# Kernel optimization log

Measured on AMD Instinct MI355X. Metric: run time of the kernel, lower is better.

## Reference

```python
import jax, jax.numpy as jnp
import numpy as np

PRE_NMS_TOP_K = 6000   # 'test' mode
POST_NMS_TOP_K = 300   # 'test' mode
IOU_THRESHOLD = 0.7


def setup_inputs() -> dict:
    key = jax.random.key(0)
    k1, k2, k3, k4 = jax.random.split(key, 4)
    B, A, H, W = 1, 9, 64, 96
    N = H * W * A  # 55296 anchors
    pred_cls = jax.random.normal(k1, (B, 2 * A, H, W), dtype=jnp.float32)
    pred_loc = jax.random.normal(k2, (B, 4 * A, H, W), dtype=jnp.float32) * 0.1
    # anchors in normalized (cx, cy, w, h) format
    cxcy = jax.random.uniform(k3, (N, 2), dtype=jnp.float32)
    wh = jax.random.uniform(k4, (N, 2), dtype=jnp.float32) * 0.2 + 0.02
    anchor = jnp.concatenate([cxcy, wh], axis=-1)
    return {"pred_cls": pred_cls, "pred_loc": pred_loc, "anchor": anchor}


def _decode_to_xy(loc, anchor):
    # decode: t(cx,cy) * a(w,h) + a(cx,cy); exp(t(w,h)) * a(w,h); then cxcy -> xyxy
    cxcy = loc[:, :2] * anchor[:, 2:] + anchor[:, :2]
    wh = jnp.exp(loc[:, 2:]) * anchor[:, 2:]
    return jnp.concatenate([cxcy - wh * 0.5, cxcy + wh * 0.5], axis=-1)


def _iou_matrix(boxes):
    # boxes: [N,4] xyxy -> [N,N] IoU
    area = (boxes[:, 2] - boxes[:, 0]) * (boxes[:, 3] - boxes[:, 1])
    lt = jnp.maximum(boxes[:, None, :2], boxes[None, :, :2])  # [N,N,2]
    rb = jnp.minimum(boxes[:, None, 2:], boxes[None, :, 2:])  # [N,N,2]
    wh = jnp.clip(rb - lt, 0.0)
    inter = wh[..., 0] * wh[..., 1]
    union = area[:, None] + area[None, :] - inter
    return inter / jnp.maximum(union, 1e-12)


def _nms_keep(boxes, iou_threshold):
    # boxes already sorted by descending score -> greedy NMS
    n = boxes.shape[0]
    iou = _iou_matrix(boxes)
    idx = jnp.arange(n)

    def body(i, keep):
        suppress = (iou[i] > iou_threshold) & (idx > i)
        return jnp.where(keep[i], keep & ~suppress, keep)

    return jax.lax.fori_loop(0, n, body, jnp.ones((n,), dtype=bool))


def reference(pred_cls, pred_loc, anchor):
    B = pred_cls.shape[0]
    # NCHW -> NHWC -> [N, 2] / [N, 4]  (batch squeezed, B == 1)
    cls = jnp.transpose(pred_cls, (0, 2, 3, 1)).reshape(B, -1, 2)[0]
    loc = jnp.transpose(pred_loc, (0, 2, 3, 1)).reshape(B, -1, 4)[0]

    roi = jnp.clip(_decode_to_xy(loc, anchor), 0.0, 1.0)           # [N,4]
    scores = jax.nn.sigmoid(cls)[:, 1]                              # [N]

    order = jnp.argsort(-scores)[:PRE_NMS_TOP_K]                    # descending
    roi = roi[order]                                                # [K,4]

    keep = _nms_keep(roi, IOU_THRESHOLD)                            # [K] bool
    # kept boxes first (stable -> preserves score order), take top 300
    sel = jnp.argsort(jnp.where(keep, 0, 1), stable=True)[:POST_NMS_TOP_K]
    valid = keep[sel]
    # pad with zeros if fewer than 300 boxes survive NMS (torch returns a
    # dynamically-sized tensor; we keep a fixed [300,4] with zero padding)
    return jnp.where(valid[:, None], roi[sel], 0.0)
```

## Files before the change

### kernel.cpp

```cpp
#include <hip/hip_runtime.h>


#define ADIM 9
#define NANCH 55296
#define HWSZ 6144
#define CH_U4 1536
#define TOT_U4 13824
#define TOPK 6000
#define OUTK 300
#define NBINS 16384
#define CAP 8192
#define SCAP 1024
#define SRANK 133
#define MROWS 512
#define MW 8
#define THR 0.7f

typedef unsigned long long u64;
typedef unsigned int u32;

__device__ __forceinline__ u32 flipu(u32 b) {
    u32 u = (b & 0x80000000u) ? ~b : (b | 0x80000000u);
    return ~u;
}

__device__ __forceinline__ bool iou_gt(float4 a, float aa, float4 b, float ba) {
    float ix = fminf(a.z, b.z) - fmaxf(a.x, b.x);
    float iy = fminf(a.w, b.w) - fmaxf(a.y, b.y);
    float inter = fmaxf(ix, 0.f) * fmaxf(iy, 0.f);
    float u = fmaxf(aa + ba - inter, 1e-12f);
    float d = __builtin_fmaf(-THR, u, inter);
    if (__builtin_fabsf(d) > 1e-6f * u) return d > 0.f;
    return inter / u > THR;
}

__device__ __forceinline__ float4 decode_box(const float* __restrict__ loc,
                                             const float* __restrict__ anc, u32 n) {
    u32 a = n % 9u, hw = n / 9u;
    float t0 = loc[(4 * a + 0) * HWSZ + hw];
    float t1 = loc[(4 * a + 1) * HWSZ + hw];
    float t2 = loc[(4 * a + 2) * HWSZ + hw];
    float t3 = loc[(4 * a + 3) * HWSZ + hw];
    float4 an = reinterpret_cast<const float4*>(anc)[n];
    float cx = t0 * an.z + an.x;
    float cy = t1 * an.w + an.y;
    float bw = expf(t2) * an.z;
    float bh = expf(t3) * an.w;
    return make_float4(fminf(fmaxf(cx - bw * 0.5f, 0.f), 1.f),
                       fminf(fmaxf(cy - bh * 0.5f, 0.f), 1.f),
                       fminf(fmaxf(cx + bw * 0.5f, 0.f), 1.f),
                       fminf(fmaxf(cy + bh * 0.5f, 0.f), 1.f));
}

__device__ __forceinline__ u64 sx64(u64 v, int m) {
    u32 lo = __shfl_xor((u32)(v & 0xffffffffu), m, 64);
    u32 hi = __shfl_xor((u32)(v >> 32), m, 64);
    return ((u64)hi << 32) | lo;
}

__device__ __forceinline__ u64 ce64(u64 v, int j, int lane, bool up) {
    u64 pv = sx64(v, j);
    u64 mn = (pv < v) ? pv : v;
    u64 mx = (pv < v) ? v : pv;
    return (((lane & j) == 0) == up) ? mn : mx;
}

__device__ __forceinline__ uint4 ld_cls4(const uint4* __restrict__ cls4, int i) {
    int ch = i / CH_U4;
    int e4 = i - ch * CH_U4;
    return cls4[(2 * ch + 1) * CH_U4 + e4];
}

__device__ __forceinline__ u32 block_scan(u32 s, int wid, int lane, u32* wsum) {
    u32 x = s;
    #pragma unroll
    for (int d = 1; d < 64; d <<= 1) {
        u32 y = __shfl_up(x, (unsigned)d, 64);
        if (lane >= d) x += y;
    }
    if (lane == 63) wsum[wid] = x;
    __syncthreads();
    if (wid == 0) {
        u32 w = (lane < 16) ? wsum[lane] : 0u;
        #pragma unroll
        for (int d = 1; d < 16; d <<= 1) {
            u32 y = __shfl_up(w, (unsigned)d, 64);
            if (lane >= d) w += y;
        }
        if (lane < 16) wsum[lane] = w;
    }
    __syncthreads();
    return x + (wid ? wsum[wid - 1] : 0u);
}

__device__ __forceinline__ u32 find_cutoff(const u32* hist, u32 thresh, int tid,
                                           int wid, int lane, u32* wsum, u32* sB) {
    u32 h[16];
    const uint4* h4 = reinterpret_cast<const uint4*>(hist);
    #pragma unroll
    for (int k = 0; k < 4; ++k) {
        uint4 v = h4[tid * 4 + k];
        h[4 * k + 0] = v.x; h[4 * k + 1] = v.y; h[4 * k + 2] = v.z; h[4 * k + 3] = v.w;
    }
    u32 s = 0;
    #pragma unroll
    for (int b = 0; b < 16; ++b) s += h[b];
    u32 incl = block_scan(s, wid, lane, wsum);
    u32 before = incl - s;
    if (before < thresh && incl >= thresh) {
        u32 run = before;
        #pragma unroll
        for (int b = 0; b < 16; ++b) {
            run += h[b];
            if (run >= thresh) { sB[0] = (u32)(tid * 16 + b); break; }
        }
    }
    __syncthreads();
    u32 r = sB[0];
    __syncthreads();
    return r;
}

__global__ void __launch_bounds__(1024) k_scanrank(const float* __restrict__ cls,
                                                   const float* __restrict__ loc,
                                                   const float* __restrict__ anc,
                                                   u32* __restrict__ wsMeta,
                                                   float4* __restrict__ boxS,
                                                   float* __restrict__ areaS) {
    __shared__ u32 hist[NBINS];
    __shared__ u64 skey[SCAP];
    __shared__ u32 wsum[16];
    __shared__ u32 sB[2];
    __shared__ u32 shu[2];

    const int tid = threadIdx.x;
    const int wid = tid >> 6;
    const int lane = tid & 63;
    const uint4* cls4 = reinterpret_cast<const uint4*>(cls);

    u64* h64 = (u64*)hist;
    for (int i = tid; i < NBINS / 2; i += 1024) h64[i] = 0ull;
    if (tid < 2) shu[tid] = 0;
    __syncthreads();

    uint4 buf[14];
    #pragma unroll
    for (int kk = 0; kk < 14; ++kk) {
        int i = kk * 1024 + tid;
        buf[kk] = (i < TOT_U4) ? ld_cls4(cls4, i)
                               : make_uint4(0xFF800000u, 0xFF800000u, 0xFF800000u, 0xFF800000u);
    }
    #pragma unroll
    for (int kk = 0; kk < 14; ++kk)
        atomicAdd(&hist[flipu(buf[kk].x) >> 18], 1u);
    __syncthreads();
    const u32 B1 = find_cutoff(hist, SRANK, tid, wid, lane, wsum, sB);
    const u32 K1 = (B1 + 1u) << 18;

    u64 bm = 0;
    u32 cnt = 0;
    #pragma unroll
    for (int kk = 0; kk < 14; ++kk) {
        int i = kk * 1024 + tid;
        if (i < TOT_U4) {
            #pragma unroll
            for (int c = 0; c < 4; ++c) {
                u32 b = (c == 0) ? buf[kk].x : (c == 1) ? buf[kk].y
                      : (c == 2) ? buf[kk].z : buf[kk].w;
                if (flipu(b) < K1) {
                    cnt++;
                    bm |= 1ull << (kk * 4 + c);
                }
            }
        }
    }
    u32 incl = block_scan(cnt, wid, lane, wsum);
    u32 base = incl - cnt;
    if (tid == 1023) shu[0] = incl;
    __syncthreads();
    const u32 csRaw = shu[0];
    const u32 cs = csRaw < SCAP ? csRaw : SCAP;
    if (blockIdx.x == 0 && tid == 0) { wsMeta[0] = csRaw; wsMeta[1] = B1; }
    if (csRaw > SCAP) return;

    {
        u64 m = bm;
        u32 o = base;
        while (m) {
            int b = __ffsll((unsigned long long)m) - 1;
            m &= m - 1;
            int kk = b >> 2, c = b & 3;
            int i = kk * 1024 + tid;
            uint4 v = ld_cls4(cls4, i);
            u32 raw = (c == 0) ? v.x : (c == 1) ? v.y : (c == 2) ? v.z : v.w;
            int ch = i / CH_U4;
            int e4 = i - ch * CH_U4;
            u32 n = (u32)((e4 * 4 + c) * ADIM + ch);
            if (o < SCAP) skey[o] = ((u64)flipu(raw) << 32) | n;
            o++;
        }
    }
    if (tid >= (int)cs) skey[tid] = ~0ull;
    __syncthreads();

    const int ci = blockIdx.x * 64 + (tid >> 4);
    const int p = tid & 15;
    const u64 myk = skey[ci];
    u32 r = 0;
    #pragma unroll 8
    for (int k = 0; k < 64; ++k) {
        int j = k * 16 + p;
        r += (skey[j] < myk) ? 1u : 0u;
    }
    r += __shfl_xor(r, 1, 64);
    r += __shfl_xor(r, 2, 64);
    r += __shfl_xor(r, 4, 64);
    r += __shfl_xor(r, 8, 64);
    if (p == 0 && (u32)ci < csRaw) {
        float4 b = decode_box(loc, anc, (u32)myk);
        boxS[r] = b;
        areaS[r] = (b.z - b.x) * (b.w - b.y);
    }
}

__global__ void __launch_bounds__(1024) k_mat(const u32* __restrict__ wsMeta,
                                              const float4* __restrict__ boxS,
                                              const float* __restrict__ areaS,
                                              u32* __restrict__ maskG32,
                                              float4* __restrict__ out) {
    __shared__ float4 B[MROWS];
    __shared__ float  A[MROWS];
    __shared__ u32 M32[32][16];
    const int tid = threadIdx.x;
    if (blockIdx.x == 0 && tid < OUTK)
        out[tid] = make_float4(0.f, 0.f, 0.f, 0.f);
    const u32 csRaw = wsMeta[0];
    if (csRaw > SCAP) return;
    const u32 rowsv = csRaw < MROWS ? csRaw : MROWS;

    if (tid < MROWS) { B[tid] = boxS[tid]; A[tid] = areaS[tid]; }
    if (tid < 512) M32[tid >> 4][tid & 15] = 0u;
    __syncthreads();

    const int rl = tid >> 5;
    const int sub = tid & 31;
    const int row = blockIdx.x + 16 * rl;
    if (row < (int)rowsv) {
        const int j0 = sub * 16;
        int jmax = row < j0 + 16 ? row : j0 + 16;
        if (j0 < jmax) {
            float4 rb = B[row];
            float rba = A[row];
            u32 bits = 0;
            #pragma unroll 4
            for (int j = j0; j < jmax; ++j)
                if (iou_gt(rb, rba, B[j], A[j])) bits |= 1u << (j - j0);
            if (bits) atomicOr(&M32[rl][sub >> 1], bits << ((sub & 1) * 16));
        }
    }
    __syncthreads();
    if (tid < 512) {
        int rl2 = tid >> 4, w = tid & 15;
        int row2 = blockIdx.x + 16 * rl2;
        maskG32[row2 * 16 + w] = M32[rl2][w];
    }
}

__global__ void __launch_bounds__(1024) k_greedy(const float* __restrict__ cls,
                                                 const float* __restrict__ loc,
                                                 const float* __restrict__ anc,
                                                 const u32* __restrict__ wsMeta,
                                                 const float4* __restrict__ boxS,
                                                 const float* __restrict__ areaS,
                                                 const u32* __restrict__ maskG32,
                                                 float4* __restrict__ out) {
    __shared__ u64 cand[CAP];
    __shared__ u64 smask[MROWS][MW];
    __shared__ float4 sbox[SCAP];
    __shared__ float  sarea[SCAP];
    __shared__ float4 kept[OUTK];
    __shared__ float  karea[OUTK];
    __shared__ float4 cbox[64];
    __shared__ float  carea[64];
    __shared__ u64 supw[16];
    __shared__ u64 sbyp[1024];
    __shared__ u32 wsum[16];
    __shared__ u32 sB[2];
    __shared__ u32 shu[8];

    const int tid = threadIdx.x;
    const int wid = tid >> 6;
    const int lane = tid & 63;
    u32* hist = (u32*)cand;
    const uint4* cls4 = reinterpret_cast<const uint4*>(cls);

    const u32 csRaw = wsMeta[0];
    const u32 cs = csRaw < SCAP ? csRaw : SCAP;
    const bool fast = (csRaw <= SCAP);

    if (tid < 8) shu[tid] = 0;
    sbox[tid] = boxS[tid];
    sarea[tid] = areaS[tid];
    {
        u32* sm32 = (u32*)smask;
        #pragma unroll
        for (int k = 0; k < 8; ++k) sm32[k * 1024 + tid] = maskG32[k * 1024 + tid];
    }
    __syncthreads();

    if (fast) {
        const u32 rowsv = cs < MROWS ? cs : MROWS;
        if (wid == 0) {
            u32 kc = 0, nexti0 = 0;
            u64 K[MW];
            #pragma unroll
            for (int w = 0; w < MW; ++w) K[w] = 0ull;
            #pragma unroll
            for (int cw = 0; cw < MW; ++cw) {
                u32 i0 = (u32)cw * 64u;
                if (i0 < rowsv && kc < OUTK) {
                    u32 ci = i0 + (u32)lane;
                    bool valid = ci < rowsv;
                    u64 myw[MW];
                    #pragma unroll
                    for (int w = 0; w < MW; ++w) myw[w] = valid ? smask[ci][w] : 0ull;
                    u64 supk = 0;
                    #pragma unroll
                    for (int w = 0; w < MW; ++w) supk |= myw[w] & K[w];
                    bool ia = valid && (supk == 0ull);
                    u64 inch = myw[cw] & ((1ull << lane) - 1ull);
                    u64 A = __ballot(ia ? 1 : 0);
                    for (int itx = 0; itx < 64; ++itx) {
                        bool na = ia && ((inch & A) == 0ull);
                        u64 A2 = __ballot(na ? 1 : 0);
                        if (A2 == A) break;
                        A = A2;
                    }
                    bool kp = (A >> lane) & 1;
                    u32 rank = (u32)__popcll(A & ((1ull << lane) - 1ull));
                    if (kp && kc + rank < OUTK) {
                        float4 c = sbox[ci];
                        kept[kc + rank] = c;
                        karea[kc + rank] = sarea[ci];
                        out[kc + rank] = c;
                    }
                    K[cw] = A;
                    kc += (u32)__popcll(A);
                    nexti0 = i0 + 64;
                }
            }
            if (lane == 0) {
                shu[4] = kc > OUTK ? OUTK : kc;
                shu[5] = nexti0;
            }
        }

        const u32 limit = cs;
        while (true) {
            __syncthreads();
            u32 kc = shu[4], i0 = shu[5];
            if (kc >= OUTK || i0 >= limit) break;
            u32 ci = i0 + (u32)lane;
            bool valid = ci < limit;
            float4 c = sbox[valid ? ci : 0];
            float ca = sarea[valid ? ci : 0];

            bool sup = false;
            for (u32 j = (u32)wid; j < kc; j += 16)
                sup = sup || iou_gt(c, ca, kept[j], karea[j]);
            u64 bal = __ballot(sup ? 1 : 0);
            if (lane == 0) supw[wid] = bal;

            u64 sby = 0;
            u32 smax = 4u * wid + 4u; if (smax > 63u) smax = 63u;
            for (u32 s = 4u * wid + 1u; s <= smax; ++s) {
                u32 p = ((u32)lane + s) & 63u;
                if (p < (u32)lane && (i0 + p) < limit)
                    if (iou_gt(c, ca, sbox[i0 + p], sarea[i0 + p])) sby |= (1ull << p);
            }
            sbyp[wid * 64 + lane] = sby;
            __syncthreads();

            if (wid == 0) {
                u64 sup64 = 0, sbyfull = 0;
                #pragma unroll
                for (int w = 0; w < 16; ++w) { sup64 |= supw[w]; sbyfull |= sbyp[w * 64 + lane]; }
                bool ia = valid && !((sup64 >> lane) & 1);
                u64 A = __ballot(ia ? 1 : 0);
                for (int itx = 0; itx < 64; ++itx) {
                    bool na = ia && ((sbyfull & A) == 0);
                    u64 A2 = __ballot(na ? 1 : 0);
                    if (A2 == A) break;
                    A = A2;
                }
                bool kp = (A >> lane) & 1;
                u32 rank = (u32)__popcll(A & ((1ull << lane) - 1ull));
                if (kp && kc + rank < OUTK) {
                    kept[kc + rank] = c; karea[kc + rank] = ca; out[kc + rank] = c;
                }
                if (lane == 0) {
                    u32 nk = kc + (u32)__popcll(A);
                    shu[4] = nk > OUTK ? OUTK : nk;
                    shu[5] = i0 + 64;
                }
            }
        }
    }

    __syncthreads();
    if (shu[4] < OUTK) {
        const u32 consumed = fast ? cs : 0u;
        u64* h64 = (u64*)hist;
        for (int i = tid; i < NBINS / 2; i += 1024) h64[i] = 0ull;
        __syncthreads();
        #pragma unroll
        for (int half = 0; half < 2; ++half) {
            uint4 buf[7];
            #pragma unroll
            for (int kk = 0; kk < 7; ++kk) {
                int i = (half * 7 + kk) * 1024 + tid;
                buf[kk] = (i < TOT_U4) ? ld_cls4(cls4, i) : make_uint4(0u,0u,0u,0u);
            }
            #pragma unroll
            for (int kk = 0; kk < 7; ++kk) {
                int i = (half * 7 + kk) * 1024 + tid;
                if (i < TOT_U4) {
                    atomicAdd(&hist[flipu(buf[kk].x) >> 18], 1u);
                    atomicAdd(&hist[flipu(buf[kk].y) >> 18], 1u);
                    atomicAdd(&hist[flipu(buf[kk].z) >> 18], 1u);
                    atomicAdd(&hist[flipu(buf[kk].w) >> 18], 1u);
                }
            }
        }
        __syncthreads();
        const u32 B2 = find_cutoff(hist, TOPK, tid, wid, lane, wsum, sB);
        u64 bm2 = 0;
        u32 cnt2 = 0;
        #pragma unroll
        for (int half = 0; half < 2; ++half) {
            uint4 buf[7];
            #pragma unroll
            for (int kk = 0; kk < 7; ++kk) {
                int i = (half * 7 + kk) * 1024 + tid;
                buf[kk] = (i < TOT_U4) ? ld_cls4(cls4, i) : make_uint4(0xFFFFFFFFu,0xFFFFFFFFu,0xFFFFFFFFu,0xFFFFFFFFu);
            }
            #pragma unroll
            for (int kk = 0; kk < 7; ++kk) {
                int i = (half * 7 + kk) * 1024 + tid;
                if (i < TOT_U4) {
                    #pragma unroll
                    for (int c = 0; c < 4; ++c) {
                        u32 b = (c == 0) ? buf[kk].x : (c == 1) ? buf[kk].y
                              : (c == 2) ? buf[kk].z : buf[kk].w;
                        if ((flipu(b) >> 18) <= B2) {
                            cnt2++;
                            bm2 |= 1ull << ((half * 7 + kk) * 4 + c);
                        }
                    }
                }
            }
        }
        __syncthreads();
        for (int i = tid; i < CAP; i += 1024) cand[i] = ~0ull;
        u32 incl2 = block_scan(cnt2, wid, lane, wsum);
        u32 base2 = incl2 - cnt2;
        if (tid == 1023) shu[1] = incl2;
        __syncthreads();
        {
            u64 m2 = bm2;
            u32 o = base2;
            while (m2) {
                int b = __ffsll((unsigned long long)m2) - 1;
                m2 &= m2 - 1;
                int kk = b >> 2, c = b & 3;
                int i = kk * 1024 + tid;
                uint4 v = ld_cls4(cls4, i);
                u32 raw = (c == 0) ? v.x : (c == 1) ? v.y : (c == 2) ? v.z : v.w;
                int ch = i / CH_U4;
                int e4 = i - ch * CH_U4;
                u32 n = (u32)((e4 * 4 + c) * ADIM + ch);
                if (o < CAP) cand[o] = ((u64)flipu(raw) << 32) | n;
                o++;
            }
        }
        __syncthreads();
        const u32 totF = shu[1];
        const u32 limfb = totF < TOPK ? totF : TOPK;
        for (int seg = wid; seg < CAP / 64; seg += 16) {
            u64 v = cand[seg * 64 + lane];
            #pragma unroll
            for (int k = 2; k <= 64; k <<= 1)
                #pragma unroll
                for (int j = k >> 1; j >= 1; j >>= 1)
                    v = ce64(v, j, lane, (((seg * 64 + lane) & k) == 0));
            cand[seg * 64 + lane] = v;
        }
        __syncthreads();
        for (int k = 128; k <= CAP; k <<= 1) {
            for (int j = k >> 1; j >= 64; j >>= 1) {
                for (u32 p = (u32)tid; p < CAP / 2; p += 1024) {
                    u32 i = ((p & ~(u32)(j - 1)) << 1) | (p & (u32)(j - 1));
                    u32 l = i | (u32)j;
                    bool up = ((i & (u32)k) == 0);
                    u64 a = cand[i], b = cand[l];
                    if ((a > b) == up) { cand[i] = b; cand[l] = a; }
                }
                __syncthreads();
            }
            for (int seg = wid; seg < CAP / 64; seg += 16) {
                u64 v = cand[seg * 64 + lane];
                bool up = (((seg * 64) & k) == 0);
                #pragma unroll
                for (int j = 32; j >= 1; j >>= 1) v = ce64(v, j, lane, up);
                cand[seg * 64 + lane] = v;
            }
            __syncthreads();
        }
        if (tid == 0) shu[5] = consumed;
        while (true) {
            __syncthreads();
            u32 kc = shu[4], i0 = shu[5];
            if (kc >= OUTK || i0 >= limfb) break;
            if (wid == 0) {
                u32 ci = i0 + (u32)lane;
                u32 n = (ci < limfb) ? (u32)cand[ci] : 0u;
                float4 b = decode_box(loc, anc, n);
                cbox[lane] = b;
                carea[lane] = (b.z - b.x) * (b.w - b.y);
            }
            __syncthreads();
            u32 ci = i0 + (u32)lane;
            bool valid = ci < limfb;
            float4 c = cbox[lane];
            float ca = carea[lane];
            bool sup = false;
            for (u32 j = (u32)wid; j < kc; j += 16)
                sup = sup || iou_gt(c, ca, kept[j], karea[j]);
            u64 bal = __ballot(sup ? 1 : 0);
            if (lane == 0) supw[wid] = bal;
            u64 sby = 0;
            u32 smax = 4u * wid + 4u; if (smax > 63u) smax = 63u;
            for (u32 s = 4u * wid + 1u; s <= smax; ++s) {
                u32 p = ((u32)lane + s) & 63u;
                if (p < (u32)lane && (i0 + p) < limfb)
                    if (iou_gt(c, ca, cbox[p], carea[p])) sby |= (1ull << p);
            }
            sbyp[wid * 64 + lane] = sby;
            __syncthreads();
            if (wid == 0) {
                u64 sup64 = 0, sbyfull = 0;
                #pragma unroll
                for (int w = 0; w < 16; ++w) { sup64 |= supw[w]; sbyfull |= sbyp[w * 64 + lane]; }
                bool ia = valid && !((sup64 >> lane) & 1);
                u64 A = __ballot(ia ? 1 : 0);
                for (int itx = 0; itx < 64; ++itx) {
                    bool na = ia && ((sbyfull & A) == 0);
                    u64 A2 = __ballot(na ? 1 : 0);
                    if (A2 == A) break;
                    A = A2;
                }
                bool kp = (A >> lane) & 1;
                u32 rank = (u32)__popcll(A & ((1ull << lane) - 1ull));
                if (kp && kc + rank < OUTK) {
                    kept[kc + rank] = c; karea[kc + rank] = ca; out[kc + rank] = c;
                }
                if (lane == 0) {
                    u32 nk = kc + (u32)__popcll(A);
                    shu[4] = nk > OUTK ? OUTK : nk;
                    shu[5] = i0 + 64;
                }
            }
        }
        __syncthreads();
        u32 kcF2 = shu[4];
        for (u32 r = (u32)tid; r < OUTK; r += 1024)
            if (r >= kcF2) out[r] = make_float4(0.f, 0.f, 0.f, 0.f);
    }
}

extern "C" void kernel_launch(void* const* d_in, const int* in_sizes, int n_in,
                              void* d_out, int out_size, void* d_ws, size_t ws_size,
                              hipStream_t stream) {
    const float* cls = (const float*)d_in[0];
    const float* loc = (const float*)d_in[1];
    const float* anc = (const float*)d_in[2];

    char* ws = (char*)d_ws;
    u32*    wsMeta  = (u32*)(ws + 0);
    float4* boxS    = (float4*)(ws + 16);
    float*  areaS   = (float*)(ws + 16400);
    u32*    maskG32 = (u32*)(ws + 20496);

    k_scanrank<<<16, 1024, 0, stream>>>(cls, loc, anc, wsMeta, boxS, areaS);
    k_mat     <<<16, 1024, 0, stream>>>(wsMeta, boxS, areaS, maskG32, (float4*)d_out);
    k_greedy  <<<1, 1024, 0, stream>>>(cls, loc, anc, wsMeta, boxS, areaS, maskG32, (float4*)d_out);
}
```

Measured before the change: 30.30 us.

## Fuse IoU-mask and greedy kernels with an atomic-counter inter-block handoff

Merges the IoU mask kernel and the single-block greedy kernel into one launch. Blocks 0-15 build the mask and then increment a global counter. The extra greedy block preloads boxes and spin-waits on that counter before reading the mask. This removes one kernel launch boundary and lets the greedy block's setup overlap with mask construction. In exchange it relies on all 17 blocks being co-resident to avoid deadlock, and it adds atomic traffic and spin-polling.

```diff
diff --git a/kernel.cpp b/kernel.cpp
--- a/kernel.cpp
+++ b/kernel.cpp
@@ -15,6 +15,7 @@
 #define MROWS 512
 #define MW 8
 #define THR 0.7f
+#define NMAT 16
 
 typedef unsigned long long u64;
 typedef unsigned int u32;
@@ -180,7 +181,9 @@
     __syncthreads();
     const u32 csRaw = shu[0];
     const u32 cs = csRaw < SCAP ? csRaw : SCAP;
-    if (blockIdx.x == 0 && tid == 0) { wsMeta[0] = csRaw; wsMeta[1] = B1; }
+    if (blockIdx.x == 0 && tid == 0) {
+        wsMeta[0] = csRaw; wsMeta[1] = B1; wsMeta[2] = 0u;
+    }
     if (csRaw > SCAP) return;
 
     {
@@ -223,57 +226,14 @@
     }
 }
 
-__global__ void __launch_bounds__(1024) k_mat(const u32* __restrict__ wsMeta,
-                                              const float4* __restrict__ boxS,
-                                              const float* __restrict__ areaS,
-                                              u32* __restrict__ maskG32,
-                                              float4* __restrict__ out) {
-    __shared__ float4 B[MROWS];
-    __shared__ float  A[MROWS];
-    __shared__ u32 M32[32][16];
-    const int tid = threadIdx.x;
-    if (blockIdx.x == 0 && tid < OUTK)
-        out[tid] = make_float4(0.f, 0.f, 0.f, 0.f);
-    const u32 csRaw = wsMeta[0];
-    if (csRaw > SCAP) return;
-    const u32 rowsv = csRaw < MROWS ? csRaw : MROWS;
-
-    if (tid < MROWS) { B[tid] = boxS[tid]; A[tid] = areaS[tid]; }
-    if (tid < 512) M32[tid >> 4][tid & 15] = 0u;
-    __syncthreads();
-
-    const int rl = tid >> 5;
-    const int sub = tid & 31;
-    const int row = blockIdx.x + 16 * rl;
-    if (row < (int)rowsv) {
-        const int j0 = sub * 16;
-        int jmax = row < j0 + 16 ? row : j0 + 16;
-        if (j0 < jmax) {
-            float4 rb = B[row];
-            float rba = A[row];
-            u32 bits = 0;
-            #pragma unroll 4
-            for (int j = j0; j < jmax; ++j)
-                if (iou_gt(rb, rba, B[j], A[j])) bits |= 1u << (j - j0);
-            if (bits) atomicOr(&M32[rl][sub >> 1], bits << ((sub & 1) * 16));
-        }
-    }
-    __syncthreads();
-    if (tid < 512) {
-        int rl2 = tid >> 4, w = tid & 15;
-        int row2 = blockIdx.x + 16 * rl2;
-        maskG32[row2 * 16 + w] = M32[rl2][w];
-    }
-}
-
-__global__ void __launch_bounds__(1024) k_greedy(const float* __restrict__ cls,
-                                                 const float* __restrict__ loc,
-                                                 const float* __restrict__ anc,
-                                                 const u32* __restrict__ wsMeta,
-                                                 const float4* __restrict__ boxS,
-                                                 const float* __restrict__ areaS,
-                                                 const u32* __restrict__ maskG32,
-                                                 float4* __restrict__ out) {
+__global__ void __launch_bounds__(1024) k_matgreedy(const float* __restrict__ cls,
+                                                    const float* __restrict__ loc,
+                                                    const float* __restrict__ anc,
+                                                    u32* __restrict__ wsMeta,
+                                                    const float4* __restrict__ boxS,
+                                                    const float* __restrict__ areaS,
+                                                    u32* __restrict__ maskG32,
+                                                    float4* __restrict__ out) {
     __shared__ u64 cand[CAP];
     __shared__ u64 smask[MROWS][MW];
     __shared__ float4 sbox[SCAP];
@@ -298,13 +258,62 @@
     const u32 cs = csRaw < SCAP ? csRaw : SCAP;
     const bool fast = (csRaw <= SCAP);
 
+    if (blockIdx.x < NMAT) {
+        if (blockIdx.x == 0 && tid < OUTK)
+            out[tid] = make_float4(0.f, 0.f, 0.f, 0.f);
+        if (fast) {
+            const u32 rowsv = csRaw < MROWS ? csRaw : MROWS;
+            u32* M32 = (u32*)sbyp;
+            if (tid < MROWS) { sbox[tid] = boxS[tid]; sarea[tid] = areaS[tid]; }
+            if (tid < 512) M32[tid] = 0u;
+            __syncthreads();
+            const int rl = tid >> 5;
+            const int sub = tid & 31;
+            const int row = blockIdx.x + 16 * rl;
+            if (row < (int)rowsv) {
+                const int j0 = sub * 16;
+                int jmax = row < j0 + 16 ? row : j0 + 16;
+                if (j0 < jmax) {
+                    float4 rb = sbox[row];
+                    float rba = sarea[row];
+                    u32 bits = 0;
+                    #pragma unroll 4
+                    for (int j = j0; j < jmax; ++j)
+                        if (iou_gt(rb, rba, sbox[j], sarea[j])) bits |= 1u << (j - j0);
+                    if (bits) atomicOr(&M32[rl * 16 + (sub >> 1)], bits << ((sub & 1) * 16));
+                }
+            }
+            __syncthreads();
+            if (tid < 512) {
+                int rl2 = tid >> 4, w = tid & 15;
+                int row2 = blockIdx.x + 16 * rl2;
+                __hip_atomic_store(&maskG32[row2 * 16 + w], M32[rl2 * 16 + w],
+                                   __ATOMIC_RELAXED, __HIP_MEMORY_SCOPE_AGENT);
+            }
+        }
+        __syncthreads();
+        if (tid == 0) {
+            __threadfence();
+            __hip_atomic_fetch_add(&wsMeta[2], 1u, __ATOMIC_RELEASE, __HIP_MEMORY_SCOPE_AGENT);
+        }
+        return;
+    }
+
     if (tid < 8) shu[tid] = 0;
     sbox[tid] = boxS[tid];
     sarea[tid] = areaS[tid];
+    if (tid == 0) {
+        u32 v;
+        do { v = __hip_atomic_load(&wsMeta[2], __ATOMIC_ACQUIRE, __HIP_MEMORY_SCOPE_AGENT); }
+        while (v < (u32)NMAT);
+    }
+    __syncthreads();
     {
         u32* sm32 = (u32*)smask;
         #pragma unroll
-        for (int k = 0; k < 8; ++k) sm32[k * 1024 + tid] = maskG32[k * 1024 + tid];
+        for (int k = 0; k < 8; ++k)
+            sm32[k * 1024 + tid] = __hip_atomic_load(&maskG32[k * 1024 + tid],
+                                                     __ATOMIC_RELAXED, __HIP_MEMORY_SCOPE_AGENT);
     }
     __syncthreads();
 
@@ -591,7 +600,7 @@
     float*  areaS   = (float*)(ws + 16400);
     u32*    maskG32 = (u32*)(ws + 20496);
 
-    k_scanrank<<<16, 1024, 0, stream>>>(cls, loc, anc, wsMeta, boxS, areaS);
-    k_mat     <<<16, 1024, 0, stream>>>(wsMeta, boxS, areaS, maskG32, (float4*)d_out);
-    k_greedy  <<<1, 1024, 0, stream>>>(cls, loc, anc, wsMeta, boxS, areaS, maskG32, (float4*)d_out);
-}
+    k_scanrank <<<16, 1024, 0, stream>>>(cls, loc, anc, wsMeta, boxS, areaS);
+    k_matgreedy<<<NMAT + 1, 1024, 0, stream>>>(cls, loc, anc, wsMeta, boxS, areaS,
+                                               maskG32, (float4*)d_out);
+}
```

Measured after the change: 31.54 us. +4.1%, slower.
